# Kernel optimization log

Measured on AMD Instinct MI355X. Metric: run time of the kernel, lower is better.

Reference implementation:

```python
import jax, jax.numpy as jnp
import numpy as np

L, N, E, H, K = 2048, 8, 2048, 8192, 8

def setup_inputs() -> dict:
    key = jax.random.key(0)
    ks = jax.random.split(key, 6)
    return {
        'x': jax.random.normal(ks[0], (L, N, E), dtype=jnp.float32),
        'proj1': jax.random.normal(ks[1], (H, E), dtype=jnp.float32) * 0.02,
        'proj1_bias': jax.random.normal(ks[2], (H,), dtype=jnp.float32) * 0.02,
        'proj2': jax.random.normal(ks[3], (E, H), dtype=jnp.float32) * 0.02,
        'proj2_bias': jax.random.normal(ks[4], (E,), dtype=jnp.float32) * 0.02,
        'gate_w': jax.random.normal(ks[5], (E, K), dtype=jnp.float32),
    }

def reference(x, proj1, proj1_bias, proj2, proj2_bias, gate_w):
    # Gating: top-1 expert per token (argmax over expert affinities).
    # NOTE: in the source, every expert applies the SAME shared proj1/proj2,
    # and recv_from_experts restores the original token order exactly, so the
    # dispatch/combine is a mathematical identity permutation. The forward
    # math is therefore exactly a shared two-layer GELU MLP on all tokens.
    dst = jnp.argmax(jnp.einsum('lne,ek->lnk', x, gate_w), axis=-1)  # [L,N] int, routing ids
    h = jax.nn.gelu(jnp.einsum('lne,he->lnh', x, proj1) + proj1_bias, approximate=False)
    out = jnp.einsum('lnh,eh->lne', h, proj2) + proj2_bias
    del dst  # routing does not affect the output (shared expert weights)
    return out
```

## Files before the change

kernel.cpp:

```cpp
#include <hip/hip_runtime.h>
#include <hip/hip_bf16.h>
#include <cstdint>
#include <cstddef>

typedef __bf16 bf16_t;
typedef __bf16 bf16x4 __attribute__((ext_vector_type(4)));
typedef __bf16 bf16x8 __attribute__((ext_vector_type(8)));
typedef float  f32x4  __attribute__((ext_vector_type(4)));

#define L_DIM 2048
#define N_DIM 8
#define E_DIM 2048
#define H_DIM 8192
#define T_DIM (L_DIM * N_DIM)

__global__ __launch_bounds__(256) void cvt_f32_bf16(const float* __restrict__ in,
                                                    bf16_t* __restrict__ out,
                                                    int n4) {
    int stride = gridDim.x * blockDim.x;
    for (int i = blockIdx.x * blockDim.x + threadIdx.x; i < n4; i += stride) {
        float4 v = *(const float4*)(in + (size_t)i * 4);
        bf16x4 o;
        o[0] = (bf16_t)v.x; o[1] = (bf16_t)v.y;
        o[2] = (bf16_t)v.z; o[3] = (bf16_t)v.w;
        *(bf16x4*)(out + (size_t)i * 4) = o;
    }
}

__device__ __forceinline__ float fast_gelu(float x) {
    float x2 = x * x;
    float w  = x * __builtin_fmaf(0.1029456f, x2, 2.3022618f);
    w = fminf(w, 60.0f);
    float s = __builtin_amdgcn_exp2f(w);
    float r = __builtin_amdgcn_rcpf(s + 1.0f);
    return x * s * r;
}

template <bool GELU_OUT>
__global__ __launch_bounds__(512, 2) void gemm256(const bf16_t* __restrict__ Am,
                                                  const bf16_t* __restrict__ Bm,
                                                  const float* __restrict__ bias,
                                                  void* __restrict__ Cout,
                                                  int M, int N, int K) {
    extern __shared__ char lds[];
    constexpr int BM = 256, BN = 256, BK = 64;
    const int NT = K / BK;

    const int tid  = threadIdx.x;
    const int lane = tid & 63;
    const int wid  = tid >> 6;
    const int wr   = wid >> 2;
    const int wc   = wid & 3;

    const int nTn = N / BN;
    const int nwg = (M / BM) * nTn;
    const int q   = nwg >> 3;
    const int wg  = (blockIdx.x & 7) * q + (blockIdx.x >> 3);
    const size_t rowBase = (size_t)(wg / nTn) * BM;
    const size_t colBase = (size_t)(wg % nTn) * BN;

    const int srow  = wid * 8 + (lane >> 3);
    const int scol8 = ((lane & 7) ^ (lane >> 3)) * 8;

    auto STAGE = [&](int isB, int half, int slot) {
        const int kt_ = (slot < NT) ? slot : (NT - 1);
        const unsigned reg_ = (unsigned)((slot & 1) * 65536 + isB * 32768 + half * 16384);
        const bf16_t* gbase_ = isB ? Bm : Am;
        const size_t gr_ = (isB ? colBase : rowBase) + (size_t)(half * 128 + srow);
        const bf16_t* s0 = gbase_ + gr_ * (size_t)K + (size_t)(kt_ * 64 + scol8);
        __builtin_amdgcn_global_load_lds(
            (const __attribute__((address_space(1))) void*)s0,
            (__attribute__((address_space(3))) void*)(lds + reg_ + (unsigned)(wid * 1024)),
            16, 0, 0);
        __builtin_amdgcn_global_load_lds(
            (const __attribute__((address_space(1))) void*)(s0 + (size_t)64 * K),
            (__attribute__((address_space(3))) void*)(lds + reg_ + (unsigned)((8 + wid) * 1024)),
            16, 0, 0);
    };

    auto ldsA = [&](unsigned bufo, int m, int kk) -> bf16x8 {
        const int row  = (m >> 1) * 64 + wr * 32 + (m & 1) * 16 + (lane & 15);
        const int slot = ((kk << 2) + (lane >> 4)) ^ (lane & 7);
        return *(const bf16x8*)(lds + bufo + row * 128 + slot * 16);
    };
    auto ldsB = [&](unsigned bufo, int n, int kk) -> bf16x8 {
        const int row  = wc * 64 + n * 16 + (lane & 15);
        const int slot = ((kk << 2) + (lane >> 4)) ^ (lane & 7);
        return *(const bf16x8*)(lds + bufo + 32768 + row * 128 + slot * 16);
    };

    f32x4 acc[8][4] = {};

    STAGE(1, 0, 0); STAGE(1, 1, 0); STAGE(0, 0, 0); STAGE(0, 1, 0);
    STAGE(1, 0, 1); STAGE(1, 1, 1); STAGE(0, 0, 1);
    asm volatile("s_waitcnt vmcnt(6)" ::: "memory");
    __builtin_amdgcn_s_barrier();

    for (int t = 0; t < NT; ++t) {
        const unsigned cur = (unsigned)(t & 1) * 65536u;
        bf16x8 bf[4][2];
        bf16x8 af[2][2];

#pragma unroll
        for (int n = 0; n < 4; ++n)
#pragma unroll
            for (int kk = 0; kk < 2; ++kk)
                bf[n][kk] = ldsB(cur, n, kk);
#pragma unroll
        for (int mm = 0; mm < 2; ++mm)
#pragma unroll
            for (int kk = 0; kk < 2; ++kk)
                af[mm][kk] = ldsA(cur, mm, kk);
        STAGE(0, 1, t + 1);
        asm volatile("s_waitcnt lgkmcnt(8)" ::: "memory");
        __builtin_amdgcn_s_barrier();
        asm volatile("s_waitcnt lgkmcnt(0)" ::: "memory");
        __builtin_amdgcn_s_setprio(1);
#pragma unroll
        for (int mm = 0; mm < 2; ++mm)
#pragma unroll
            for (int n = 0; n < 4; ++n)
#pragma unroll
                for (int kk = 0; kk < 2; ++kk)
                    acc[mm][n] = __builtin_amdgcn_mfma_f32_16x16x32_bf16(
                        af[mm][kk], bf[n][kk], acc[mm][n], 0, 0, 0);
        __builtin_amdgcn_s_setprio(0);
        __builtin_amdgcn_s_barrier();

#pragma unroll
        for (int ph = 1; ph < 4; ++ph) {
#pragma unroll
            for (int mm = 0; mm < 2; ++mm)
#pragma unroll
                for (int kk = 0; kk < 2; ++kk)
                    af[mm][kk] = ldsA(cur, ph * 2 + mm, kk);
            if (ph == 1)      STAGE(1, 0, t + 2);
            else if (ph == 2) STAGE(1, 1, t + 2);
            else {            STAGE(0, 0, t + 2);
                              asm volatile("s_waitcnt vmcnt(6)" ::: "memory"); }
            __builtin_amdgcn_s_barrier();
            asm volatile("s_waitcnt lgkmcnt(0)" ::: "memory");
            __builtin_amdgcn_s_setprio(1);
#pragma unroll
            for (int mm = 0; mm < 2; ++mm)
#pragma unroll
                for (int n = 0; n < 4; ++n)
#pragma unroll
                    for (int kk = 0; kk < 2; ++kk)
                        acc[ph * 2 + mm][n] = __builtin_amdgcn_mfma_f32_16x16x32_bf16(
                            af[mm][kk], bf[n][kk], acc[ph * 2 + mm][n], 0, 0, 0);
            __builtin_amdgcn_s_setprio(0);
            __builtin_amdgcn_s_barrier();
        }
    }
    asm volatile("s_waitcnt vmcnt(0)" ::: "memory");

    const int orow = (lane >> 4) * 4;
    const int ocol = lane & 15;
#pragma unroll
    for (int m = 0; m < 8; ++m) {
        const size_t rb = rowBase + (size_t)((m >> 1) * 64 + wr * 32 + (m & 1) * 16 + orow);
#pragma unroll
        for (int n = 0; n < 4; ++n) {
            const size_t col = colBase + (size_t)(wc * 64 + n * 16 + ocol);
            const float bv = bias[col];
#pragma unroll
            for (int j = 0; j < 4; ++j) {
                float v = acc[m][n][j] + bv;
                if constexpr (GELU_OUT) {
                    ((bf16_t*)Cout)[(rb + j) * (size_t)N + col] = (bf16_t)fast_gelu(v);
                } else {
                    ((float*)Cout)[(rb + j) * (size_t)N + col] = v;
                }
            }
        }
    }
}

extern "C" void kernel_launch(void* const* d_in, const int* in_sizes, int n_in,
                              void* d_out, int out_size, void* d_ws, size_t ws_size,
                              hipStream_t stream) {
    const float* x  = (const float*)d_in[0];
    const float* p1 = (const float*)d_in[1];
    const float* b1 = (const float*)d_in[2];
    const float* p2 = (const float*)d_in[3];
    const float* b2 = (const float*)d_in[4];
    float* out = (float*)d_out;

    char* ws = (char*)d_ws;
    bf16_t* xb  = (bf16_t*)(ws);
    bf16_t* p1b = (bf16_t*)(ws + ((size_t)64 << 20));
    bf16_t* p2b = (bf16_t*)(ws + ((size_t)96 << 20));
    bf16_t* h   = (bf16_t*)(ws + ((size_t)128 << 20));

    (void)hipFuncSetAttribute((const void*)gemm256<true>,
                              hipFuncAttributeMaxDynamicSharedMemorySize, 131072);
    (void)hipFuncSetAttribute((const void*)gemm256<false>,
                              hipFuncAttributeMaxDynamicSharedMemorySize, 131072);

    cvt_f32_bf16<<<2048, 256, 0, stream>>>(x,  xb,  (T_DIM * E_DIM) / 4);
    cvt_f32_bf16<<<1024, 256, 0, stream>>>(p1, p1b, (H_DIM * E_DIM) / 4);
    cvt_f32_bf16<<<1024, 256, 0, stream>>>(p2, p2b, (E_DIM * H_DIM) / 4);

    gemm256<true><<<(T_DIM / 256) * (H_DIM / 256), 512, 131072, stream>>>(
        xb, p1b, b1, (void*)h, T_DIM, H_DIM, E_DIM);

    gemm256<false><<<(T_DIM / 256) * (E_DIM / 256), 512, 131072, stream>>>(
        h, p2b, b2, (void*)out, T_DIM, E_DIM, H_DIM);
}
```

Baseline: 1.075 ms.

## Make GEMM kernels persistent with 256 workgroups looping over multiple tiles

Both GEMMs now launch exactly 256 workgroups. Each workgroup processes several consecutive 256x256 output tiles (8 for the first GEMM, 2 for the second), and the global-to-LDS prefetch pipeline runs continuously across tile boundaries. The epilogue runs per tile and resets the accumulators. This removes wave-quantization tails and per-workgroup launch and prologue costs, and keeps the prefetch flowing between tiles. In exchange, the tile order and L2 locality change, and the epilogue stores now sit inside the main loop.

Result: no change. 1.059 ms (-1.5%).

```diff
diff --git a/kernel.cpp b/kernel.cpp
--- a/kernel.cpp
+++ b/kernel.cpp
@@ -41,10 +41,12 @@
                                                   const bf16_t* __restrict__ Bm,
                                                   const float* __restrict__ bias,
                                                   void* __restrict__ Cout,
-                                                  int M, int N, int K) {
+                                                  int N, int K,
+                                                  int lgNT, int lgTn, int lgNtile) {
     extern __shared__ char lds[];
-    constexpr int BM = 256, BN = 256, BK = 64;
-    const int NT = K / BK;
+    const int NT    = 1 << lgNT;
+    const int ntile = 1 << lgNtile;
+    const int U     = ntile << lgNT;
 
     const int tid  = threadIdx.x;
     const int lane = tid & 63;
@@ -52,22 +54,21 @@
     const int wr   = wid >> 2;
     const int wc   = wid & 3;
 
-    const int nTn = N / BN;
-    const int nwg = (M / BM) * nTn;
-    const int q   = nwg >> 3;
-    const int wg  = (blockIdx.x & 7) * q + (blockIdx.x >> 3);
-    const size_t rowBase = (size_t)(wg / nTn) * BM;
-    const size_t colBase = (size_t)(wg % nTn) * BN;
+    const int wgb = (blockIdx.x & 7) * 32 + (blockIdx.x >> 3);
 
     const int srow  = wid * 8 + (lane >> 3);
     const int scol8 = ((lane & 7) ^ (lane >> 3)) * 8;
 
     auto STAGE = [&](int isB, int half, int slot) {
-        const int kt_ = (slot < NT) ? slot : (NT - 1);
-        const unsigned reg_ = (unsigned)((slot & 1) * 65536 + isB * 32768 + half * 16384);
-        const bf16_t* gbase_ = isB ? Bm : Am;
-        const size_t gr_ = (isB ? colBase : rowBase) + (size_t)(half * 128 + srow);
-        const bf16_t* s0 = gbase_ + gr_ * (size_t)K + (size_t)(kt_ * 64 + scol8);
+        const int us  = (slot < U) ? slot : (U - 1);
+        const int ti_ = us >> lgNT;
+        const int kt_ = us & (NT - 1);
+        const int g_  = (wgb << lgNtile) + ti_;
+        const size_t base_ = (size_t)(isB ? (g_ & ((1 << lgTn) - 1)) : (g_ >> lgTn)) << 8;
+        const unsigned reg_ = (unsigned)(((slot & 1) << 16) | (isB << 15) | (half << 14));
+        const bf16_t* s0 = (isB ? Bm : Am)
+                         + (base_ + (size_t)(half * 128 + srow)) * (size_t)K
+                         + (size_t)((kt_ << 6) + scol8);
         __builtin_amdgcn_global_load_lds(
             (const __attribute__((address_space(1))) void*)s0,
             (__attribute__((address_space(3))) void*)(lds + reg_ + (unsigned)(wid * 1024)),
@@ -96,48 +97,25 @@
     asm volatile("s_waitcnt vmcnt(6)" ::: "memory");
     __builtin_amdgcn_s_barrier();
 
-    for (int t = 0; t < NT; ++t) {
-        const unsigned cur = (unsigned)(t & 1) * 65536u;
-        bf16x8 bf[4][2];
-        bf16x8 af[2][2];
-
-#pragma unroll
-        for (int n = 0; n < 4; ++n)
-#pragma unroll
-            for (int kk = 0; kk < 2; ++kk)
-                bf[n][kk] = ldsB(cur, n, kk);
-#pragma unroll
-        for (int mm = 0; mm < 2; ++mm)
-#pragma unroll
-            for (int kk = 0; kk < 2; ++kk)
-                af[mm][kk] = ldsA(cur, mm, kk);
-        STAGE(0, 1, t + 1);
-        asm volatile("s_waitcnt lgkmcnt(8)" ::: "memory");
-        __builtin_amdgcn_s_barrier();
-        asm volatile("s_waitcnt lgkmcnt(0)" ::: "memory");
-        __builtin_amdgcn_s_setprio(1);
-#pragma unroll
-        for (int mm = 0; mm < 2; ++mm)
+    for (int ti = 0; ti < ntile; ++ti) {
+        for (int t = 0; t < NT; ++t) {
+            const int u = (ti << lgNT) + t;
+            const unsigned cur = (unsigned)(t & 1) * 65536u;
+            bf16x8 bf[4][2];
+            bf16x8 af[2][2];
+
 #pragma unroll
             for (int n = 0; n < 4; ++n)
 #pragma unroll
                 for (int kk = 0; kk < 2; ++kk)
-                    acc[mm][n] = __builtin_amdgcn_mfma_f32_16x16x32_bf16(
-                        af[mm][kk], bf[n][kk], acc[mm][n], 0, 0, 0);
-        __builtin_amdgcn_s_setprio(0);
-        __builtin_amdgcn_s_barrier();
-
-#pragma unroll
-        for (int ph = 1; ph < 4; ++ph) {
+                    bf[n][kk] = ldsB(cur, n, kk);
 #pragma unroll
             for (int mm = 0; mm < 2; ++mm)
 #pragma unroll
                 for (int kk = 0; kk < 2; ++kk)
-                    af[mm][kk] = ldsA(cur, ph * 2 + mm, kk);
-            if (ph == 1)      STAGE(1, 0, t + 2);
-            else if (ph == 2) STAGE(1, 1, t + 2);
-            else {            STAGE(0, 0, t + 2);
-                              asm volatile("s_waitcnt vmcnt(6)" ::: "memory"); }
+                    af[mm][kk] = ldsA(cur, mm, kk);
+            STAGE(0, 1, u + 1);
+            asm volatile("s_waitcnt lgkmcnt(8)" ::: "memory");
             __builtin_amdgcn_s_barrier();
             asm volatile("s_waitcnt lgkmcnt(0)" ::: "memory");
             __builtin_amdgcn_s_setprio(1);
@@ -147,34 +125,64 @@
                 for (int n = 0; n < 4; ++n)
 #pragma unroll
                     for (int kk = 0; kk < 2; ++kk)
-                        acc[ph * 2 + mm][n] = __builtin_amdgcn_mfma_f32_16x16x32_bf16(
-                            af[mm][kk], bf[n][kk], acc[ph * 2 + mm][n], 0, 0, 0);
+                        acc[mm][n] = __builtin_amdgcn_mfma_f32_16x16x32_bf16(
+                            af[mm][kk], bf[n][kk], acc[mm][n], 0, 0, 0);
             __builtin_amdgcn_s_setprio(0);
             __builtin_amdgcn_s_barrier();
+
+#pragma unroll
+            for (int ph = 1; ph < 4; ++ph) {
+#pragma unroll
+                for (int mm = 0; mm < 2; ++mm)
+#pragma unroll
+                    for (int kk = 0; kk < 2; ++kk)
+                        af[mm][kk] = ldsA(cur, ph * 2 + mm, kk);
+                if (ph == 1)      STAGE(1, 0, u + 2);
+                else if (ph == 2) STAGE(1, 1, u + 2);
+                else {            STAGE(0, 0, u + 2);
+                                  asm volatile("s_waitcnt vmcnt(6)" ::: "memory"); }
+                __builtin_amdgcn_s_barrier();
+                asm volatile("s_waitcnt lgkmcnt(0)" ::: "memory");
+                __builtin_amdgcn_s_setprio(1);
+#pragma unroll
+                for (int mm = 0; mm < 2; ++mm)
+#pragma unroll
+                    for (int n = 0; n < 4; ++n)
+#pragma unroll
+                        for (int kk = 0; kk < 2; ++kk)
+                            acc[ph * 2 + mm][n] = __builtin_amdgcn_mfma_f32_16x16x32_bf16(
+                                af[mm][kk], bf[n][kk], acc[ph * 2 + mm][n], 0, 0, 0);
+                __builtin_amdgcn_s_setprio(0);
+                __builtin_amdgcn_s_barrier();
+            }
+        }
+
+        const int g = (wgb << lgNtile) + ti;
+        const size_t rowBase = (size_t)(g >> lgTn) << 8;
+        const size_t colBase = (size_t)(g & ((1 << lgTn) - 1)) << 8;
+        const int orow = (lane >> 4) * 4;
+        const int ocol = lane & 15;
+#pragma unroll
+        for (int m = 0; m < 8; ++m) {
+            const size_t rb = rowBase + (size_t)((m >> 1) * 64 + wr * 32 + (m & 1) * 16 + orow);
+#pragma unroll
+            for (int n = 0; n < 4; ++n) {
+                const size_t col = colBase + (size_t)(wc * 64 + n * 16 + ocol);
+                const float bv = bias[col];
+#pragma unroll
+                for (int j = 0; j < 4; ++j) {
+                    float v = acc[m][n][j] + bv;
+                    if constexpr (GELU_OUT) {
+                        ((bf16_t*)Cout)[(rb + j) * (size_t)N + col] = (bf16_t)fast_gelu(v);
+                    } else {
+                        ((float*)Cout)[(rb + j) * (size_t)N + col] = v;
+                    }
+                }
+                acc[m][n] = (f32x4){0.f, 0.f, 0.f, 0.f};
+            }
         }
     }
     asm volatile("s_waitcnt vmcnt(0)" ::: "memory");
-
-    const int orow = (lane >> 4) * 4;
-    const int ocol = lane & 15;
-#pragma unroll
-    for (int m = 0; m < 8; ++m) {
-        const size_t rb = rowBase + (size_t)((m >> 1) * 64 + wr * 32 + (m & 1) * 16 + orow);
-#pragma unroll
-        for (int n = 0; n < 4; ++n) {
-            const size_t col = colBase + (size_t)(wc * 64 + n * 16 + ocol);
-            const float bv = bias[col];
-#pragma unroll
-            for (int j = 0; j < 4; ++j) {
-                float v = acc[m][n][j] + bv;
-                if constexpr (GELU_OUT) {
-                    ((bf16_t*)Cout)[(rb + j) * (size_t)N + col] = (bf16_t)fast_gelu(v);
-                } else {
-                    ((float*)Cout)[(rb + j) * (size_t)N + col] = v;
-                }
-            }
-        }
-    }
 }
 
 extern "C" void kernel_launch(void* const* d_in, const int* in_sizes, int n_in,
@@ -202,9 +210,9 @@
     cvt_f32_bf16<<<1024, 256, 0, stream>>>(p1, p1b, (H_DIM * E_DIM) / 4);
     cvt_f32_bf16<<<1024, 256, 0, stream>>>(p2, p2b, (E_DIM * H_DIM) / 4);
 
-    gemm256<true><<<(T_DIM / 256) * (H_DIM / 256), 512, 131072, stream>>>(
-        xb, p1b, b1, (void*)h, T_DIM, H_DIM, E_DIM);
-
-    gemm256<false><<<(T_DIM / 256) * (E_DIM / 256), 512, 131072, stream>>>(
-        h, p2b, b2, (void*)out, T_DIM, E_DIM, H_DIM);
-}
+    gemm256<true><<<256, 512, 131072, stream>>>(
+        xb, p1b, b1, (void*)h, H_DIM, E_DIM, 5, 5, 3);
+
+    gemm256<false><<<256, 512, 131072, stream>>>(
+        h, p2b, b2, (void*)out, E_DIM, H_DIM, 7, 3, 1);
+}
```
